# Kernel tuning notes

Measured on AMD Instinct MI355X. Metric: run time of the kernel, lower is better.

## Reference

```python
import jax, jax.numpy as jnp
import numpy as np


def _bfp_quantize_blocks(x, mantissa, blk):
    """x: [..., C] fp; quantize each contiguous block of `blk` channels to a
    shared-exponent block floating point format with `mantissa` mantissa bits."""
    lead = x.shape[:-1]
    C = x.shape[-1]
    xb = x.reshape(lead + (C // blk, blk))
    max_abs = jnp.max(jnp.abs(xb), axis=-1, keepdims=True)
    # frexp: max_abs = f * 2**e with f in [0.5, 1)  =>  floor(log2(max_abs)) = e - 1
    _, e = jnp.frexp(max_abs)
    shared_exp = e - 1
    # quantization step so mantissa magnitude fits in `mantissa` bits
    quantum = jnp.exp2((shared_exp - (mantissa - 1)).astype(x.dtype))
    lim = jnp.asarray(2.0 ** mantissa - 1.0, dtype=x.dtype)
    q = jnp.clip(jnp.round(xb / quantum), -lim, lim) * quantum
    q = jnp.where(max_abs > 0, q, jnp.zeros_like(q))  # all-zero block -> 0
    return q.reshape(lead + (C,))


def setup_inputs() -> dict:
    key = jax.random.key(0)
    activations = jax.random.normal(key, (8, 64, 32, 64, 64), dtype=jnp.float32)
    return {"activations": activations, "mantissa": 7, "blk": 16}


def reference(activations, mantissa, blk):
    # permute=True path: blocks are along the channel dim C of [N, C, D, H, W]
    x = jnp.transpose(activations, (0, 2, 3, 4, 1))  # [N, D, H, W, C]
    q = _bfp_quantize_blocks(x, mantissa, blk)
    return jnp.transpose(q, (0, 4, 1, 2, 3))  # back to [N, C, D, H, W]
```

## Files before the change

### kernel.cpp

```cpp
#include <hip/hip_runtime.h>
#include <math.h>

#define CH_STRIDE 131072
#define SPATIAL4  32768
#define NBLK      32
#define BLK       16

__global__ __launch_bounds__(256)
void bfp_quant_kernel(const float* __restrict__ in, float* __restrict__ out) {
    const int tid = blockIdx.x * blockDim.x + threadIdx.x;
    const int sp4 = tid & (SPATIAL4 - 1);
    const int nb  = tid >> 15;

    const long base = (long)nb * (long)(BLK * CH_STRIDE) + (long)sp4 * 4;
    const float4* __restrict__ ip = (const float4*)(in  + base);
    float4*       __restrict__ op = (float4*)(out + base);

    float v[BLK][4];
    float mx0 = 0.f, mx1 = 0.f, mx2 = 0.f, mx3 = 0.f;

    #pragma unroll
    for (int c = 0; c < BLK; ++c) {
        float4 t = ip[c * SPATIAL4];
        v[c][0] = t.x; v[c][1] = t.y; v[c][2] = t.z; v[c][3] = t.w;
        mx0 = fmaxf(mx0, fabsf(t.x));
        mx1 = fmaxf(mx1, fabsf(t.y));
        mx2 = fmaxf(mx2, fabsf(t.z));
        mx3 = fmaxf(mx3, fabsf(t.w));
    }

    int e0, e1, e2, e3;
    (void)frexpf(mx0, &e0); (void)frexpf(mx1, &e1);
    (void)frexpf(mx2, &e2); (void)frexpf(mx3, &e3);
    const float q0 = ldexpf(1.0f, e0 - 7), i0 = ldexpf(1.0f, 7 - e0);
    const float q1 = ldexpf(1.0f, e1 - 7), i1 = ldexpf(1.0f, 7 - e1);
    const float q2 = ldexpf(1.0f, e2 - 7), i2 = ldexpf(1.0f, 7 - e2);
    const float q3 = ldexpf(1.0f, e3 - 7), i3 = ldexpf(1.0f, 7 - e3);

    const float lim = 127.0f;

    #pragma unroll
    for (int c = 0; c < BLK; ++c) {
        float4 r;
        r.x = fminf(fmaxf(rintf(v[c][0] * i0), -lim), lim) * q0;
        r.y = fminf(fmaxf(rintf(v[c][1] * i1), -lim), lim) * q1;
        r.z = fminf(fmaxf(rintf(v[c][2] * i2), -lim), lim) * q2;
        r.w = fminf(fmaxf(rintf(v[c][3] * i3), -lim), lim) * q3;
        op[c * SPATIAL4] = r;
    }
}

extern "C" void kernel_launch(void* const* d_in, const int* in_sizes, int n_in,
                              void* d_out, int out_size, void* d_ws, size_t ws_size,
                              hipStream_t stream) {
    const float* in  = (const float*)d_in[0];
    float*       out = (float*)d_out;
    const int threads = 256;
    const int blocks  = (NBLK * SPATIAL4) / threads;
    bfp_quant_kernel<<<blocks, threads, 0, stream>>>(in, out);
}
```

Measured before the change: 426.3 us.

## Split each channel block across four lanes with wave shuffle max reduction

Each thread now loads only four channels of a 16-channel block instead of all sixteen, and the block max is combined across four lanes with xor shuffles. This quadruples the thread count and cuts per-thread register use, aiming for higher occupancy and more memory requests in flight on a bandwidth-bound kernel. Each wave's accesses become four 256-byte segments rather than one 1KB contiguous run, and it adds shuffle instructions.

```diff
diff --git a/kernel.cpp b/kernel.cpp
--- a/kernel.cpp
+++ b/kernel.cpp
@@ -3,51 +3,74 @@
 
 #define CH_STRIDE 131072
 #define SPATIAL4  32768
-#define NBLK      32
 #define BLK       16
 
 __global__ __launch_bounds__(256)
 void bfp_quant_kernel(const float* __restrict__ in, float* __restrict__ out) {
-    const int tid = blockIdx.x * blockDim.x + threadIdx.x;
-    const int sp4 = tid & (SPATIAL4 - 1);
-    const int nb  = tid >> 15;
+    const int tid   = blockIdx.x * 256 + threadIdx.x;
+    const int lane  = threadIdx.x & 63;
+    const int sp    = lane & 15;
+    const int ch2   = lane >> 4;
+    const int wid   = tid >> 6;
+    const int chunk = wid & 2047;
+    const int nb    = wid >> 11;
+    const int sp4   = (chunk << 4) + sp;
 
-    const long base = (long)nb * (long)(BLK * CH_STRIDE) + (long)sp4 * 4;
+    const long base = (long)nb * (BLK * (long)CH_STRIDE)
+                    + (long)(ch2 * 4) * CH_STRIDE
+                    + (long)sp4 * 4;
     const float4* __restrict__ ip = (const float4*)(in  + base);
     float4*       __restrict__ op = (float4*)(out + base);
 
-    float v[BLK][4];
-    float mx0 = 0.f, mx1 = 0.f, mx2 = 0.f, mx3 = 0.f;
+    const float4 v0 = ip[0];
+    const float4 v1 = ip[SPATIAL4];
+    const float4 v2 = ip[2 * SPATIAL4];
+    const float4 v3 = ip[3 * SPATIAL4];
 
-    #pragma unroll
-    for (int c = 0; c < BLK; ++c) {
-        float4 t = ip[c * SPATIAL4];
-        v[c][0] = t.x; v[c][1] = t.y; v[c][2] = t.z; v[c][3] = t.w;
-        mx0 = fmaxf(mx0, fabsf(t.x));
-        mx1 = fmaxf(mx1, fabsf(t.y));
-        mx2 = fmaxf(mx2, fabsf(t.z));
-        mx3 = fmaxf(mx3, fabsf(t.w));
-    }
+    float mx = fmaxf(fmaxf(fabsf(v0.x), fabsf(v1.x)), fmaxf(fabsf(v2.x), fabsf(v3.x)));
+    float my = fmaxf(fmaxf(fabsf(v0.y), fabsf(v1.y)), fmaxf(fabsf(v2.y), fabsf(v3.y)));
+    float mz = fmaxf(fmaxf(fabsf(v0.z), fabsf(v1.z)), fmaxf(fabsf(v2.z), fabsf(v3.z)));
+    float mw = fmaxf(fmaxf(fabsf(v0.w), fabsf(v1.w)), fmaxf(fabsf(v2.w), fabsf(v3.w)));
 
-    int e0, e1, e2, e3;
-    (void)frexpf(mx0, &e0); (void)frexpf(mx1, &e1);
-    (void)frexpf(mx2, &e2); (void)frexpf(mx3, &e3);
-    const float q0 = ldexpf(1.0f, e0 - 7), i0 = ldexpf(1.0f, 7 - e0);
-    const float q1 = ldexpf(1.0f, e1 - 7), i1 = ldexpf(1.0f, 7 - e1);
-    const float q2 = ldexpf(1.0f, e2 - 7), i2 = ldexpf(1.0f, 7 - e2);
-    const float q3 = ldexpf(1.0f, e3 - 7), i3 = ldexpf(1.0f, 7 - e3);
+    mx = fmaxf(mx, __shfl_xor(mx, 16, 64));
+    my = fmaxf(my, __shfl_xor(my, 16, 64));
+    mz = fmaxf(mz, __shfl_xor(mz, 16, 64));
+    mw = fmaxf(mw, __shfl_xor(mw, 16, 64));
+    mx = fmaxf(mx, __shfl_xor(mx, 32, 64));
+    my = fmaxf(my, __shfl_xor(my, 32, 64));
+    mz = fmaxf(mz, __shfl_xor(mz, 32, 64));
+    mw = fmaxf(mw, __shfl_xor(mw, 32, 64));
 
+    int ex, ey, ez, ew;
+    (void)frexpf(mx, &ex); (void)frexpf(my, &ey);
+    (void)frexpf(mz, &ez); (void)frexpf(mw, &ew);
+    const float qx = ldexpf(1.0f, ex - 7), rx = ldexpf(1.0f, 7 - ex);
+    const float qy = ldexpf(1.0f, ey - 7), ry = ldexpf(1.0f, 7 - ey);
+    const float qz = ldexpf(1.0f, ez - 7), rz = ldexpf(1.0f, 7 - ez);
+    const float qw = ldexpf(1.0f, ew - 7), rw = ldexpf(1.0f, 7 - ew);
     const float lim = 127.0f;
 
-    #pragma unroll
-    for (int c = 0; c < BLK; ++c) {
-        float4 r;
-        r.x = fminf(fmaxf(rintf(v[c][0] * i0), -lim), lim) * q0;
-        r.y = fminf(fmaxf(rintf(v[c][1] * i1), -lim), lim) * q1;
-        r.z = fminf(fmaxf(rintf(v[c][2] * i2), -lim), lim) * q2;
-        r.w = fminf(fmaxf(rintf(v[c][3] * i3), -lim), lim) * q3;
-        op[c * SPATIAL4] = r;
-    }
+    float4 o;
+    o.x = fminf(fmaxf(rintf(v0.x * rx), -lim), lim) * qx;
+    o.y = fminf(fmaxf(rintf(v0.y * ry), -lim), lim) * qy;
+    o.z = fminf(fmaxf(rintf(v0.z * rz), -lim), lim) * qz;
+    o.w = fminf(fmaxf(rintf(v0.w * rw), -lim), lim) * qw;
+    op[0] = o;
+    o.x = fminf(fmaxf(rintf(v1.x * rx), -lim), lim) * qx;
+    o.y = fminf(fmaxf(rintf(v1.y * ry), -lim), lim) * qy;
+    o.z = fminf(fmaxf(rintf(v1.z * rz), -lim), lim) * qz;
+    o.w = fminf(fmaxf(rintf(v1.w * rw), -lim), lim) * qw;
+    op[SPATIAL4] = o;
+    o.x = fminf(fmaxf(rintf(v2.x * rx), -lim), lim) * qx;
+    o.y = fminf(fmaxf(rintf(v2.y * ry), -lim), lim) * qy;
+    o.z = fminf(fmaxf(rintf(v2.z * rz), -lim), lim) * qz;
+    o.w = fminf(fmaxf(rintf(v2.w * rw), -lim), lim) * qw;
+    op[2 * SPATIAL4] = o;
+    o.x = fminf(fmaxf(rintf(v3.x * rx), -lim), lim) * qx;
+    o.y = fminf(fmaxf(rintf(v3.y * ry), -lim), lim) * qy;
+    o.z = fminf(fmaxf(rintf(v3.z * rz), -lim), lim) * qz;
+    o.w = fminf(fmaxf(rintf(v3.w * rw), -lim), lim) * qw;
+    op[3 * SPATIAL4] = o;
 }
 
 extern "C" void kernel_launch(void* const* d_in, const int* in_sizes, int n_in,
@@ -55,7 +78,5 @@
                               hipStream_t stream) {
     const float* in  = (const float*)d_in[0];
     float*       out = (float*)d_out;
-    const int threads = 256;
-    const int blocks  = (NBLK * SPATIAL4) / threads;
-    bfp_quant_kernel<<<blocks, threads, 0, stream>>>(in, out);
+    bfp_quant_kernel<<<16384, 256, 0, stream>>>(in, out);
 }
```

Result: no change. 426.1 us (-0.0%).
